# Performance work log

Hardware: AMD Instinct MI355X
Metric: run time of the kernel (lower is better)

The kernel has to match this reference:

```python
import jax, jax.numpy as jnp
import numpy as np

EPS = 1e-5


def setup_inputs() -> dict:
    key = jax.random.key(0)
    k1, k2, k3 = jax.random.split(key, 3)
    B, C, H, W = 32, 64, 32, 32
    N = 16  # out_planes: number of independent BatchNorm2d branches
    x = jax.random.normal(k1, (B, C, H, W), dtype=jnp.float32)
    # per-branch affine params (torch init is gamma=1, beta=0; randomize for testing)
    gamma = jax.random.uniform(k2, (N, C), dtype=jnp.float32, minval=0.5, maxval=1.5)
    beta = jax.random.normal(k3, (N, C), dtype=jnp.float32) * 0.1
    return {"x": x, "gamma": gamma, "beta": beta}


def reference(x, gamma, beta):
    # All N BatchNorm2d branches see the identical input, so the batch
    # mean/var reduction over (B, H, W) is computed ONCE and shared.
    mean = jnp.mean(x, axis=(0, 2, 3))                    # [C]
    var = jnp.mean((x - mean[None, :, None, None]) ** 2,  # biased var, as torch BN
                   axis=(0, 2, 3))                        # [C]
    inv = jax.lax.rsqrt(var + EPS)                        # [C]
    xhat = (x - mean[None, :, None, None]) * inv[None, :, None, None]  # [B,C,H,W]
    # Per-branch affine, then concat along channel dim -> [B, N*C, H, W]
    out = gamma[None, :, :, None, None] * xhat[:, None] + beta[None, :, :, None, None]
    B, N, C, H, W = out.shape
    return out.reshape(B, N * C, H, W)
```

## Files before the change

### kernel.cpp

```cpp
#include <hip/hip_runtime.h>

#define CH      64
#define BATCH   32
#define NBR     16
#define HW4     256

typedef float v4f __attribute__((ext_vector_type(4)));

__global__ void __launch_bounds__(256) bn_partial(const float* __restrict__ x,
                                                  float* __restrict__ partials) {
    const int b    = blockIdx.x & 31;
    const int cg   = blockIdx.x >> 5;
    const int wave = threadIdx.x >> 6;
    const int lane = threadIdx.x & 63;
    const int c    = cg * 4 + wave;

    const v4f* xp = (const v4f*)x + (b * CH + c) * HW4;
    float s = 0.f, sq = 0.f;
#pragma unroll
    for (int i = 0; i < 4; ++i) {
        const v4f v = xp[i * 64 + lane];
        s  += v.x + v.y + v.z + v.w;
        sq += v.x * v.x + v.y * v.y + v.z * v.z + v.w * v.w;
    }
#pragma unroll
    for (int off = 32; off > 0; off >>= 1) {
        s  += __shfl_down(s, off);
        sq += __shfl_down(sq, off);
    }
    if (lane == 0) {
        partials[(b * CH + c) * 2 + 0] = s;
        partials[(b * CH + c) * 2 + 1] = sq;
    }
}

__global__ void __launch_bounds__(256) bn_apply(const float* __restrict__ x,
                                                const float* __restrict__ partials,
                                                const float* __restrict__ gamma,
                                                const float* __restrict__ beta,
                                                float* __restrict__ out) {
    const int bid  = blockIdx.x;
    const int b    = bid & 31;
    const int n    = (bid >> 5) & 15;
    const int half = bid >> 9;
    const int t    = threadIdx.x;

    __shared__ float sa[32], ss[32];
    if (t < 32) {
        const int c = half * 32 + t;
        float S = 0.f, Q = 0.f;
#pragma unroll
        for (int bb = 0; bb < 32; ++bb) {
            S += partials[(bb * CH + c) * 2 + 0];
            Q += partials[(bb * CH + c) * 2 + 1];
        }
        const float mean = S * (1.0f / 32768.0f);
        const float var  = Q * (1.0f / 32768.0f) - mean * mean;
        const float inv  = rsqrtf(var + 1e-5f);
        const float a    = gamma[n * CH + c] * inv;
        sa[t] = a;
        ss[t] = beta[n * CH + c] - a * mean;
    }
    __syncthreads();

    const v4f* xp = (const v4f*)x   + (b * CH + half * 32) * HW4 + t;
    v4f*       op = (v4f*)out + ((b * NBR + n) * CH + half * 32) * HW4 + t;
#pragma unroll 4
    for (int cc = 0; cc < 32; ++cc) {
        const float a = sa[cc];
        const float s = ss[cc];
        const v4f v = xp[cc * HW4];
        v4f o;
        o.x = fmaf(a, v.x, s);
        o.y = fmaf(a, v.y, s);
        o.z = fmaf(a, v.z, s);
        o.w = fmaf(a, v.w, s);
        __builtin_nontemporal_store(o, &op[cc * HW4]);
    }
}

extern "C" void kernel_launch(void* const* d_in, const int* in_sizes, int n_in,
                              void* d_out, int out_size, void* d_ws, size_t ws_size,
                              hipStream_t stream) {
    const float* x     = (const float*)d_in[0];
    const float* gamma = (const float*)d_in[1];
    const float* beta  = (const float*)d_in[2];
    float* out = (float*)d_out;
    float* ws  = (float*)d_ws;

    float* partials = ws;

    bn_partial<<<512, 256, 0, stream>>>(x, partials);
    bn_apply  <<<1024, 256, 0, stream>>>(x, partials, gamma, beta, out);
}
```

Baseline: 152.9 us.

## Remap apply kernel to 8 channels per block with per-thread contiguous chunks

Restructures the apply kernel so each block covers 8 channels of one (batch, branch) slice and each thread loads 8 consecutive float4 values into registers before writing them. The grid grows fourfold to raise parallelism and memory-level parallelism per thread. Nontemporal stores are replaced with ordinary stores. Per-thread contiguous access makes wavefront accesses strided, and per-block stat recomputation is repeated more often.

```diff
diff --git a/kernel.cpp b/kernel.cpp
--- a/kernel.cpp
+++ b/kernel.cpp
@@ -39,15 +39,15 @@
                                                 const float* __restrict__ gamma,
                                                 const float* __restrict__ beta,
                                                 float* __restrict__ out) {
-    const int bid  = blockIdx.x;
-    const int b    = bid & 31;
-    const int n    = (bid >> 5) & 15;
-    const int half = bid >> 9;
-    const int t    = threadIdx.x;
+    const int t     = threadIdx.x;
+    const int bbase = blockIdx.x << 11;
+    const int b     = bbase >> 18;
+    const int n     = (bbase >> 14) & 15;
+    const int c0    = (bbase >> 8) & 63;
 
-    __shared__ float sa[32], ss[32];
-    if (t < 32) {
-        const int c = half * 32 + t;
+    __shared__ float sa[8], ss[8];
+    if (t < 8) {
+        const int c = c0 + t;
         float S = 0.f, Q = 0.f;
 #pragma unroll
         for (int bb = 0; bb < 32; ++bb) {
@@ -63,19 +63,25 @@
     }
     __syncthreads();
 
-    const v4f* xp = (const v4f*)x   + (b * CH + half * 32) * HW4 + t;
-    v4f*       op = (v4f*)out + ((b * NBR + n) * CH + half * 32) * HW4 + t;
-#pragma unroll 4
-    for (int cc = 0; cc < 32; ++cc) {
-        const float a = sa[cc];
-        const float s = ss[cc];
-        const v4f v = xp[cc * HW4];
+    const int lc  = (t * 8) >> 8;
+    const int hw4 = (t * 8) & 255;
+    const float a = sa[lc];
+    const float s = ss[lc];
+
+    const v4f* xp = (const v4f*)x + (b * CH + c0 + lc) * HW4 + hw4;
+    v4f*       op = (v4f*)out + bbase + t * 8;
+
+    v4f v[8];
+#pragma unroll
+    for (int k = 0; k < 8; ++k) v[k] = xp[k];
+#pragma unroll
+    for (int k = 0; k < 8; ++k) {
         v4f o;
-        o.x = fmaf(a, v.x, s);
-        o.y = fmaf(a, v.y, s);
-        o.z = fmaf(a, v.z, s);
-        o.w = fmaf(a, v.w, s);
-        __builtin_nontemporal_store(o, &op[cc * HW4]);
+        o.x = fmaf(a, v[k].x, s);
+        o.y = fmaf(a, v[k].y, s);
+        o.z = fmaf(a, v[k].z, s);
+        o.w = fmaf(a, v[k].w, s);
+        op[k] = o;
     }
 }
 
@@ -91,5 +97,5 @@
     float* partials = ws;
 
     bn_partial<<<512, 256, 0, stream>>>(x, partials);
-    bn_apply  <<<1024, 256, 0, stream>>>(x, partials, gamma, beta, out);
+    bn_apply  <<<4096, 256, 0, stream>>>(x, partials, gamma, beta, out);
 }
```

Result: slower. 175.0 us (+14.4%).

## Fuse stats and apply kernels with a grid-wide atomic barrier

Applied to the files above, without the earlier changes.

Merges the partial-statistics kernel and the apply kernel into one launch. Each block first reduces two channels of one batch image, then all blocks wait at a software grid barrier built on a global atomic counter before reading the partials and writing the output. This removes one kernel launch and its gap, but depends on all 1024 blocks being resident at once (launch bounds of 4 blocks per SM) and adds spin-wait cost. The output stores also change from nontemporal to normal stores.

```diff
diff --git a/kernel.cpp b/kernel.cpp
--- a/kernel.cpp
+++ b/kernel.cpp
@@ -1,51 +1,77 @@
 #include <hip/hip_runtime.h>
 
-#define CH      64
-#define BATCH   32
-#define NBR     16
-#define HW4     256
+#define CH   64
+#define NBR  16
+#define HW4  256
 
 typedef float v4f __attribute__((ext_vector_type(4)));
 
-__global__ void __launch_bounds__(256) bn_partial(const float* __restrict__ x,
-                                                  float* __restrict__ partials) {
-    const int b    = blockIdx.x & 31;
-    const int cg   = blockIdx.x >> 5;
-    const int wave = threadIdx.x >> 6;
-    const int lane = threadIdx.x & 63;
-    const int c    = cg * 4 + wave;
+__device__ int g_ctr;
 
-    const v4f* xp = (const v4f*)x + (b * CH + c) * HW4;
-    float s = 0.f, sq = 0.f;
-#pragma unroll
-    for (int i = 0; i < 4; ++i) {
-        const v4f v = xp[i * 64 + lane];
-        s  += v.x + v.y + v.z + v.w;
-        sq += v.x * v.x + v.y * v.y + v.z * v.z + v.w * v.w;
-    }
-#pragma unroll
-    for (int off = 32; off > 0; off >>= 1) {
-        s  += __shfl_down(s, off);
-        sq += __shfl_down(sq, off);
-    }
-    if (lane == 0) {
-        partials[(b * CH + c) * 2 + 0] = s;
-        partials[(b * CH + c) * 2 + 1] = sq;
-    }
-}
-
-__global__ void __launch_bounds__(256) bn_apply(const float* __restrict__ x,
-                                                const float* __restrict__ partials,
-                                                const float* __restrict__ gamma,
-                                                const float* __restrict__ beta,
-                                                float* __restrict__ out) {
+__global__ void __launch_bounds__(256, 4)
+bn_fused(const float* __restrict__ x,
+         const float* __restrict__ gamma,
+         const float* __restrict__ beta,
+         float* __restrict__ partials,
+         float* __restrict__ out) {
     const int bid  = blockIdx.x;
     const int b    = bid & 31;
-    const int n    = (bid >> 5) & 15;
+    const int pair = bid >> 5;
+    const int n    = pair & 15;
     const int half = bid >> 9;
     const int t    = threadIdx.x;
+    const int wave = t >> 6, lane = t & 63;
 
+    __shared__ float ls[4][4];
     __shared__ float sa[32], ss[32];
+
+    {
+        const v4f* xp = (const v4f*)x + (b * CH + pair * 2) * HW4;
+        const v4f v0 = xp[t];
+        const v4f v1 = xp[t + 256];
+        float s0 = v0.x + v0.y + v0.z + v0.w;
+        float q0 = v0.x * v0.x + v0.y * v0.y + v0.z * v0.z + v0.w * v0.w;
+        float s1 = v1.x + v1.y + v1.z + v1.w;
+        float q1 = v1.x * v1.x + v1.y * v1.y + v1.z * v1.z + v1.w * v1.w;
+#pragma unroll
+        for (int off = 32; off > 0; off >>= 1) {
+            s0 += __shfl_down(s0, off);
+            q0 += __shfl_down(q0, off);
+            s1 += __shfl_down(s1, off);
+            q1 += __shfl_down(q1, off);
+        }
+        if (lane == 0) {
+            ls[wave][0] = s0; ls[wave][1] = q0;
+            ls[wave][2] = s1; ls[wave][3] = q1;
+        }
+        __syncthreads();
+        if (t == 0) {
+            float S0 = 0.f, Q0 = 0.f, S1 = 0.f, Q1 = 0.f;
+#pragma unroll
+            for (int w = 0; w < 4; ++w) {
+                S0 += ls[w][0]; Q0 += ls[w][1];
+                S1 += ls[w][2]; Q1 += ls[w][3];
+            }
+            const int c0 = pair * 2;
+            partials[(b * CH + c0)     * 2 + 0] = S0;
+            partials[(b * CH + c0)     * 2 + 1] = Q0;
+            partials[(b * CH + c0 + 1) * 2 + 0] = S1;
+            partials[(b * CH + c0 + 1) * 2 + 1] = Q1;
+        }
+    }
+
+    __threadfence();
+    __syncthreads();
+    if (t == 0) {
+        const int old = __hip_atomic_fetch_add(&g_ctr, 1, __ATOMIC_ACQ_REL,
+                                               __HIP_MEMORY_SCOPE_AGENT);
+        const int target = (old - (old & 1023)) + 1024;
+        while (__hip_atomic_load(&g_ctr, __ATOMIC_ACQUIRE,
+                                 __HIP_MEMORY_SCOPE_AGENT) < target)
+            __builtin_amdgcn_s_sleep(2);
+    }
+    __syncthreads();
+
     if (t < 32) {
         const int c = half * 32 + t;
         float S = 0.f, Q = 0.f;
@@ -75,7 +101,7 @@
         o.y = fmaf(a, v.y, s);
         o.z = fmaf(a, v.z, s);
         o.w = fmaf(a, v.w, s);
-        __builtin_nontemporal_store(o, &op[cc * HW4]);
+        op[cc * HW4] = o;
     }
 }
 
@@ -90,6 +116,5 @@
 
     float* partials = ws;
 
-    bn_partial<<<512, 256, 0, stream>>>(x, partials);
-    bn_apply  <<<1024, 256, 0, stream>>>(x, partials, gamma, beta, out);
+    bn_fused<<<1024, 256, 0, stream>>>(x, gamma, beta, partials, out);
 }
```

Result: slower. 231.2 us (+51.2%).
